# Kernel optimization log

Measured on AMD Instinct MI355X. Metric: run time of the kernel, lower is better.

## Reference

```python
import jax, jax.numpy as jnp
import numpy as np

N, E, G = 100000, 1600000, 64
IN, H, OUT = 128, 64, 16  # hidden/2 = 32
SLOPE = 0.01


def setup_inputs() -> dict:
    key = jax.random.key(0)
    ks = jax.random.split(key, 7)
    features = jax.random.normal(ks[0], (N, IN), dtype=jnp.float32)
    src = jax.random.randint(ks[1], (E,), 0, N)
    dst = jax.random.randint(ks[2], (E,), 0, N)
    graph_ids = jnp.sort(jax.random.randint(ks[3], (N,), 0, G))
    # kaiming-uniform-ish fan_in init, bias=False everywhere
    W1 = jax.random.uniform(ks[4], (IN, H), jnp.float32, -1.0, 1.0) * np.sqrt(3.0 / IN)
    W2 = jax.random.uniform(ks[5], (H, H // 2), jnp.float32, -1.0, 1.0) * np.sqrt(3.0 / H)
    Wc = jax.random.uniform(ks[6], (H // 2, OUT), jnp.float32, -1.0, 1.0) * np.sqrt(3.0 / (H // 2))
    return {"features": features, "src": src, "dst": dst, "graph_ids": graph_ids,
            "W1": W1, "W2": W2, "Wc": Wc}


def _graph_conv(x, W, src, dst, n):
    # DGL GraphConv, norm='both', bias=False:
    # out = D_in^{-1/2} A (D_out^{-1/2} x) W   (degrees clamped to >= 1)
    ones = jnp.ones(src.shape[0], dtype=x.dtype)
    outdeg = jnp.clip(jax.ops.segment_sum(ones, src, num_segments=n), 1.0)
    indeg = jnp.clip(jax.ops.segment_sum(ones, dst, num_segments=n), 1.0)
    h = (x * jax.lax.rsqrt(outdeg)[:, None]) @ W  # project first (in_dim > out_dim)
    m = jax.ops.segment_sum(h[src], dst, num_segments=n)  # sparse aggregation
    return m * jax.lax.rsqrt(indeg)[:, None]


def reference(features, src, dst, graph_ids, W1, W2, Wc):
    h = jax.nn.leaky_relu(_graph_conv(features, W1, src, dst, N), SLOPE)
    h = jax.nn.leaky_relu(_graph_conv(h, W2, src, dst, N), SLOPE)
    # dropout is identity at inference
    sums = jax.ops.segment_sum(h, graph_ids, num_segments=G)
    cnts = jnp.clip(jax.ops.segment_sum(jnp.ones((N,), h.dtype), graph_ids, num_segments=G), 1.0)
    mean = sums / cnts[:, None]  # dgl.mean_nodes
    return mean @ Wc  # [G, OUT]
```

## Files before the change

kernel.cpp:

```cpp
#include <hip/hip_runtime.h>

#define NN 100000
#define NE 1600000
#define NG 64
#define D_IN 128
#define D_H 64
#define D_H2 32
#define D_OUT 16
#define SLOPE 0.01f
#define REC 48

#define BSH 9
#define NBK 196
#define NCB 250
#define CHE (NE / NCB)
#define BCAP 9216

typedef _Float16 half2v __attribute__((ext_vector_type(2)));
typedef _Float16 h8 __attribute__((ext_vector_type(8)));
typedef float f32x4 __attribute__((ext_vector_type(4)));

__global__ __launch_bounds__(256) void p12_scatter(const int* __restrict__ src,
                                                   const int* __restrict__ dst,
                                                   int* __restrict__ gcur,
                                                   unsigned* __restrict__ pk,
                                                   unsigned short* __restrict__ srcs16) {
  __shared__ int hD[NBK], hS[NBK];
  __shared__ int cD[NBK], cS[NBK];
  int b = blockIdx.x, t = threadIdx.x;
  for (int i = t; i < NBK; i += 256) { hD[i] = 0; hS[i] = 0; }
  __syncthreads();
  const int4* s4 = (const int4*)(src + b * CHE);
  const int4* d4 = (const int4*)(dst + b * CHE);
  for (int i = t; i < CHE / 4; i += 256) {
    int4 s = s4[i], d = d4[i];
    atomicAdd(&hD[d.x >> BSH], 1); atomicAdd(&hD[d.y >> BSH], 1);
    atomicAdd(&hD[d.z >> BSH], 1); atomicAdd(&hD[d.w >> BSH], 1);
    atomicAdd(&hS[s.x >> BSH], 1); atomicAdd(&hS[s.y >> BSH], 1);
    atomicAdd(&hS[s.z >> BSH], 1); atomicAdd(&hS[s.w >> BSH], 1);
  }
  __syncthreads();
  for (int i = t; i < NBK; i += 256) {
    cD[i] = atomicAdd(&gcur[i], hD[i]);
    cS[i] = atomicAdd(&gcur[NBK + i], hS[i]);
  }
  __syncthreads();
  for (int i = t; i < CHE / 4; i += 256) {
    int4 s = s4[i], d = d4[i];
#pragma unroll
    for (int j = 0; j < 4; ++j) {
      int ss = (j == 0) ? s.x : (j == 1) ? s.y : (j == 2) ? s.z : s.w;
      int dd = (j == 0) ? d.x : (j == 1) ? d.y : (j == 2) ? d.z : d.w;
      int kd = dd >> BSH, ks = ss >> BSH;
      int pd = atomicAdd(&cD[kd], 1);
      if (pd < BCAP) pk[(size_t)kd * BCAP + pd] =
          ((unsigned)(dd & 511) << 17) | (unsigned)ss;
      int ps = atomicAdd(&cS[ks], 1);
      if (ps < BCAP) srcs16[(size_t)ks * BCAP + ps] = (unsigned short)(ss & 511);
    }
  }
}

__global__ __launch_bounds__(256) void p3_build(const unsigned* __restrict__ pk,
                                                const unsigned short* __restrict__ srcs16,
                                                const int* __restrict__ gcur,
                                                int* __restrict__ adj,
                                                int* __restrict__ indeg,
                                                int* __restrict__ outdeg) {
  __shared__ int hh[512];
  int bb = blockIdx.x, t = threadIdx.x;
  for (int i = t; i < 512; i += 256) hh[i] = 0;
  __syncthreads();
  if (bb < NBK) {
    int k = bb;
    int n0 = k << BSH;
    int lo = k * BCAP;
    int hi = lo + min(gcur[k], BCAP);
    for (int i = lo + t; i < hi; i += 256) {
      unsigned v = pk[i];
      int local = v >> 17;
      int pos = atomicAdd(&hh[local], 1);
      if (pos < REC) adj[(size_t)(n0 + local) * REC + pos] = (int)(v & 0x1FFFF);
    }
    __syncthreads();
    for (int i = t; i < 512; i += 256) {
      int n = n0 + i;
      if (n < NN) {
        int dg = hh[i];
        indeg[n] = dg;
        int d = min(dg, REC);
        int dr = min((d + 15) & ~15, REC);
        for (int j = d; j < dr; ++j) adj[(size_t)n * REC + j] = NN;
      }
    }
  } else {
    int k = bb - NBK;
    int lo = k * BCAP;
    int hi = lo + min(gcur[NBK + k], BCAP);
    for (int i = lo + t; i < hi; i += 256) atomicAdd(&hh[srcs16[i]], 1);
    __syncthreads();
    int n0 = k << BSH;
    for (int i = t; i < 512; i += 256) {
      int n = n0 + i;
      if (n < NN) outdeg[n] = hh[i];
    }
  }
}

__global__ __launch_bounds__(256) void k_mm1f(const float* __restrict__ X,
                                              const float* __restrict__ W,
                                              const int* __restrict__ odeg,
                                              _Float16* __restrict__ Y) {
  __shared__ _Float16 Wt[64][136];
  int t = threadIdx.x;
  if (blockIdx.x == 0 && t < 64) Y[(size_t)NN * 64 + t] = (_Float16)0.f;
  for (int i = t; i < 128 * 64; i += 256) {
    int k = i >> 6, f = i & 63;
    Wt[f][k] = (_Float16)W[i];
  }
  __syncthreads();
  int lane = t & 63, w = t >> 6;
  int m = lane & 15, q = lane >> 4;
  h8 bf[4][4];
#pragma unroll
  for (int kc = 0; kc < 4; ++kc)
#pragma unroll
    for (int nt = 0; nt < 4; ++nt)
      bf[kc][nt] = *(const h8*)&Wt[nt * 16 + m][kc * 32 + q * 8];

  const int NT = NN / 16;
  int idx = blockIdx.x * 4 + w;
  int t0 = idx * 2, t1 = t0 + 1;
  f32x4 r0[8], r1[8];
  if (t0 < NT) {
    const f32x4* X0 = (const f32x4*)(X + (size_t)(t0 * 16 + m) * 128);
#pragma unroll
    for (int kc = 0; kc < 4; ++kc) {
      r0[kc * 2 + 0] = X0[kc * 8 + q * 2 + 0];
      r0[kc * 2 + 1] = X0[kc * 8 + q * 2 + 1];
    }
  }
  if (t1 < NT) {
    const f32x4* X1 = (const f32x4*)(X + (size_t)(t1 * 16 + m) * 128);
#pragma unroll
    for (int kc = 0; kc < 4; ++kc) {
      r1[kc * 2 + 0] = X1[kc * 8 + q * 2 + 0];
      r1[kc * 2 + 1] = X1[kc * 8 + q * 2 + 1];
    }
  }
#pragma unroll
  for (int half = 0; half < 2; ++half) {
    int tile = (half == 0) ? t0 : t1;
    if (tile >= NT) continue;
    f32x4* rr = (half == 0) ? r0 : r1;
    f32x4 acc[4] = {{0,0,0,0},{0,0,0,0},{0,0,0,0},{0,0,0,0}};
#pragma unroll
    for (int kc = 0; kc < 4; ++kc) {
      f32x4 x0 = rr[kc * 2 + 0], x1 = rr[kc * 2 + 1];
      h8 a;
      a[0] = (_Float16)x0.x; a[1] = (_Float16)x0.y;
      a[2] = (_Float16)x0.z; a[3] = (_Float16)x0.w;
      a[4] = (_Float16)x1.x; a[5] = (_Float16)x1.y;
      a[6] = (_Float16)x1.z; a[7] = (_Float16)x1.w;
#pragma unroll
      for (int nt = 0; nt < 4; ++nt)
        acc[nt] = __builtin_amdgcn_mfma_f32_16x16x32_f16(a, bf[kc][nt], acc[nt], 0, 0, 0);
    }
    int n0 = tile * 16;
#pragma unroll
    for (int reg = 0; reg < 4; ++reg) {
      int nn = n0 + q * 4 + reg;
      float sc = rsqrtf((float)max(odeg[nn], 1));
#pragma unroll
      for (int nt = 0; nt < 4; ++nt)
        Y[(size_t)nn * 64 + nt * 16 + m] = (_Float16)(acc[nt][reg] * sc);
    }
  }
}

__global__ __launch_bounds__(256) void k_aggmm2(const int* __restrict__ adj,
                                                const int* __restrict__ indeg,
                                                const int* __restrict__ odeg,
                                                const h8* __restrict__ H8,
                                                const float* __restrict__ W,
                                                _Float16* __restrict__ Y) {
  __shared__ _Float16 Ht[32][72];
  __shared__ _Float16 Wt[32][72];
  int t = threadIdx.x;
  if (blockIdx.x == 0 && t < 32) Y[(size_t)NN * 32 + t] = (_Float16)0.f;
  for (int i = t; i < 64 * 32; i += 256) {
    int k = i >> 5, f = i & 31;
    Wt[f][k] = (_Float16)W[i];
  }
  int l8 = t & 7;
  int nd = t >> 3;
  int node = blockIdx.x * 32 + nd;
  int deg = indeg[node];
  int groups = (min(deg, REC) + 15) >> 4;
  const int4* c4 = (const int4*)(adj + (size_t)node * REC);
  float acc[8] = {0.f, 0.f, 0.f, 0.f, 0.f, 0.f, 0.f, 0.f};
  for (int g = 0; g < groups; ++g) {
    int4 ca = c4[g * 4 + 0], cb = c4[g * 4 + 1];
    {
      h8 v0 = H8[(size_t)ca.x * 8 + l8];
      h8 v1 = H8[(size_t)ca.y * 8 + l8];
      h8 v2 = H8[(size_t)ca.z * 8 + l8];
      h8 v3 = H8[(size_t)ca.w * 8 + l8];
      h8 v4 = H8[(size_t)cb.x * 8 + l8];
      h8 v5 = H8[(size_t)cb.y * 8 + l8];
      h8 v6 = H8[(size_t)cb.z * 8 + l8];
      h8 v7 = H8[(size_t)cb.w * 8 + l8];
#pragma unroll
      for (int j = 0; j < 8; ++j)
        acc[j] += (((float)v0[j] + (float)v1[j]) + ((float)v2[j] + (float)v3[j])) +
                  (((float)v4[j] + (float)v5[j]) + ((float)v6[j] + (float)v7[j]));
    }
    int4 cc = c4[g * 4 + 2], cd = c4[g * 4 + 3];
    {
      h8 v0 = H8[(size_t)cc.x * 8 + l8];
      h8 v1 = H8[(size_t)cc.y * 8 + l8];
      h8 v2 = H8[(size_t)cc.z * 8 + l8];
      h8 v3 = H8[(size_t)cc.w * 8 + l8];
      h8 v4 = H8[(size_t)cd.x * 8 + l8];
      h8 v5 = H8[(size_t)cd.y * 8 + l8];
      h8 v6 = H8[(size_t)cd.z * 8 + l8];
      h8 v7 = H8[(size_t)cd.w * 8 + l8];
#pragma unroll
      for (int j = 0; j < 8; ++j)
        acc[j] += (((float)v0[j] + (float)v1[j]) + ((float)v2[j] + (float)v3[j])) +
                  (((float)v4[j] + (float)v5[j]) + ((float)v6[j] + (float)v7[j]));
    }
  }
  float sc = rsqrtf((float)max(deg, 1));
  h8 hv;
#pragma unroll
  for (int j = 0; j < 8; ++j) {
    float x = acc[j] * sc;
    hv[j] = (_Float16)((x > 0.f) ? x : SLOPE * x);
  }
  *(h8*)&Ht[nd][l8 * 8] = hv;
  __syncthreads();
  int lane = t & 63, w = t >> 6;
  if (w < 2) {
    int m = lane & 15, q = lane >> 4;
    h8 bf[2][2];
#pragma unroll
    for (int kc = 0; kc < 2; ++kc)
#pragma unroll
      for (int nt = 0; nt < 2; ++nt)
        bf[kc][nt] = *(const h8*)&Wt[nt * 16 + m][kc * 32 + q * 8];
    h8 af[2];
#pragma unroll
    for (int kc = 0; kc < 2; ++kc)
      af[kc] = *(const h8*)&Ht[w * 16 + m][kc * 32 + q * 8];
    f32x4 acc2[2] = {{0, 0, 0, 0}, {0, 0, 0, 0}};
#pragma unroll
    for (int kc = 0; kc < 2; ++kc)
#pragma unroll
      for (int nt = 0; nt < 2; ++nt)
        acc2[nt] = __builtin_amdgcn_mfma_f32_16x16x32_f16(af[kc], bf[kc][nt], acc2[nt], 0, 0, 0);
#pragma unroll
    for (int reg = 0; reg < 4; ++reg) {
      int nn = blockIdx.x * 32 + w * 16 + q * 4 + reg;
      float sco = rsqrtf((float)max(odeg[nn], 1));
#pragma unroll
      for (int nt = 0; nt < 2; ++nt)
        Y[(size_t)nn * 32 + nt * 16 + m] = (_Float16)(acc2[nt][reg] * sco);
    }
  }
}

__global__ __launch_bounds__(256) void k_agg32v(const int* __restrict__ adj,
                                                const int* __restrict__ indeg,
                                                const h8* __restrict__ H8,
                                                h8* __restrict__ Y8) {
  int l4 = threadIdx.x & 3;
  int node = blockIdx.x * 64 + (threadIdx.x >> 2);
  if (node >= NN) return;
  int deg = indeg[node];
  int groups = (min(deg, REC) + 15) >> 4;
  const int4* c4 = (const int4*)(adj + (size_t)node * REC);
  float acc[8] = {0.f, 0.f, 0.f, 0.f, 0.f, 0.f, 0.f, 0.f};
  for (int g = 0; g < groups; ++g) {
    int4 ca = c4[g * 4 + 0], cb = c4[g * 4 + 1];
    {
      h8 v0 = H8[(size_t)ca.x * 4 + l4];
      h8 v1 = H8[(size_t)ca.y * 4 + l4];
      h8 v2 = H8[(size_t)ca.z * 4 + l4];
      h8 v3 = H8[(size_t)ca.w * 4 + l4];
      h8 v4 = H8[(size_t)cb.x * 4 + l4];
      h8 v5 = H8[(size_t)cb.y * 4 + l4];
      h8 v6 = H8[(size_t)cb.z * 4 + l4];
      h8 v7 = H8[(size_t)cb.w * 4 + l4];
#pragma unroll
      for (int j = 0; j < 8; ++j)
        acc[j] += (((float)v0[j] + (float)v1[j]) + ((float)v2[j] + (float)v3[j])) +
                  (((float)v4[j] + (float)v5[j]) + ((float)v6[j] + (float)v7[j]));
    }
    int4 cc = c4[g * 4 + 2], cd = c4[g * 4 + 3];
    {
      h8 v0 = H8[(size_t)cc.x * 4 + l4];
      h8 v1 = H8[(size_t)cc.y * 4 + l4];
      h8 v2 = H8[(size_t)cc.z * 4 + l4];
      h8 v3 = H8[(size_t)cc.w * 4 + l4];
      h8 v4 = H8[(size_t)cd.x * 4 + l4];
      h8 v5 = H8[(size_t)cd.y * 4 + l4];
      h8 v6 = H8[(size_t)cd.z * 4 + l4];
      h8 v7 = H8[(size_t)cd.w * 4 + l4];
#pragma unroll
      for (int j = 0; j < 8; ++j)
        acc[j] += (((float)v0[j] + (float)v1[j]) + ((float)v2[j] + (float)v3[j])) +
                  (((float)v4[j] + (float)v5[j]) + ((float)v6[j] + (float)v7[j]));
    }
  }
  float sc = rsqrtf((float)max(deg, 1));
  h8 o;
#pragma unroll
  for (int j = 0; j < 8; ++j) {
    float x = acc[j] * sc;
    o[j] = (_Float16)((x > 0.f) ? x : SLOPE * x);
  }
  Y8[(size_t)node * 4 + l4] = o;
}

__global__ __launch_bounds__(256) void k_poolout(const half2v* __restrict__ H2,
                                                 const int* __restrict__ gid,
                                                 const float* __restrict__ Wc,
                                                 float* __restrict__ out) {
  __shared__ float red[16][33];
  __shared__ float mean[D_H2];
  __shared__ int sb[2];
  int g = blockIdx.x, t = threadIdx.x;
  if (t < 2) {
    int target = g + t;
    int lo = 0, hi = NN;
    while (lo < hi) {
      int mid = (lo + hi) >> 1;
      if (gid[mid] < target) lo = mid + 1; else hi = mid;
    }
    sb[t] = lo;
  }
  __syncthreads();
  int start = sb[0], end = sb[1];
  int c2 = t & 15, r = t >> 4;
  float sx = 0.f, sy = 0.f;
  for (int n = start + r; n < end; n += 16) {
    half2v v = H2[(size_t)n * 16 + c2];
    sx += (float)v.x;
    sy += (float)v.y;
  }
  red[r][c2 * 2] = sx;
  red[r][c2 * 2 + 1] = sy;
  __syncthreads();
  if (r < 8) { red[r][c2 * 2] += red[r + 8][c2 * 2]; red[r][c2 * 2 + 1] += red[r + 8][c2 * 2 + 1]; }
  __syncthreads();
  if (r < 4) { red[r][c2 * 2] += red[r + 4][c2 * 2]; red[r][c2 * 2 + 1] += red[r + 4][c2 * 2 + 1]; }
  __syncthreads();
  if (r < 2) { red[r][c2 * 2] += red[r + 2][c2 * 2]; red[r][c2 * 2 + 1] += red[r + 2][c2 * 2 + 1]; }
  __syncthreads();
  if (r == 0) {
    float inv = 1.0f / (float)max(end - start, 1);
    mean[c2 * 2] = (red[0][c2 * 2] + red[1][c2 * 2]) * inv;
    mean[c2 * 2 + 1] = (red[0][c2 * 2 + 1] + red[1][c2 * 2 + 1]) * inv;
  }
  __syncthreads();
  if (t < D_OUT) {
    float acc = 0.f;
#pragma unroll
    for (int cc = 0; cc < D_H2; ++cc) acc += mean[cc] * Wc[cc * D_OUT + t];
    out[g * D_OUT + t] = acc;
  }
}

extern "C" void kernel_launch(void* const* d_in, const int* in_sizes, int n_in,
                              void* d_out, int out_size, void* d_ws, size_t ws_size,
                              hipStream_t stream) {
  const float* X  = (const float*)d_in[0];
  const int*   src = (const int*)d_in[1];
  const int*   dst = (const int*)d_in[2];
  const int*   gid = (const int*)d_in[3];
  const float* W1 = (const float*)d_in[4];
  const float* W2 = (const float*)d_in[5];
  const float* Wc = (const float*)d_in[6];
  float* out = (float*)d_out;

  char* p = (char*)d_ws;
  auto alloc = [&](size_t bytes) {
    char* q = p;
    p += (bytes + 255) & ~(size_t)255;
    return q;
  };
  int*            outdeg = (int*)alloc(NN * 4);
  int*            indeg  = (int*)alloc(NN * 4);
  int*            gcur   = (int*)alloc(2 * NBK * 4);
  unsigned*       pk     = (unsigned*)alloc((size_t)NBK * BCAP * 4);
  unsigned short* srcs16 = (unsigned short*)alloc((size_t)NBK * BCAP * 2);
  int*            adj    = (int*)alloc((size_t)NN * REC * 4);
  _Float16*       bufA   = (_Float16*)alloc((size_t)(NN + 1) * 64 * 2);
  _Float16*       bufB   = (_Float16*)alloc((size_t)(NN + 1) * 32 * 2);
  _Float16*       bufC   = (_Float16*)alloc((size_t)(NN + 1) * 32 * 2);

  hipMemsetAsync(gcur, 0, 2 * NBK * 4, stream);

  p12_scatter<<<NCB, 256, 0, stream>>>(src, dst, gcur, pk, srcs16);
  p3_build<<<2 * NBK, 256, 0, stream>>>(pk, srcs16, gcur, adj, indeg, outdeg);

  k_mm1f<<<782, 256, 0, stream>>>(X, W1, outdeg, bufA);
  k_aggmm2<<<NN / 32, 256, 0, stream>>>(adj, indeg, outdeg, (const h8*)bufA, W2, bufC);
  k_agg32v<<<(NN + 63) / 64, 256, 0, stream>>>(adj, indeg, (const h8*)bufC, (h8*)bufB);

  k_poolout<<<NG, 256, 0, stream>>>((const half2v*)bufB, gid, Wc, out);
}
```

Baseline: 237.1 us.

## Fuse second-layer aggregation with per-graph mean pooling via shared atomics

The final aggregation kernel now accumulates its leaky-ReLU outputs straight into per-graph sums. It uses LDS atomics across up to four graph slots per block, then global atomics into a small pool buffer, which removes the fp16 intermediate write and the separate pooling pass. A single-block kernel then computes means and the classifier matmul, and the pool buffer is zeroed by extending the existing memset. Separately, placeholder padding in the adjacency build now uses int4 stores. The fusion relies on sorted graph ids spanning at most four graphs per 64-node block, since it clamps otherwise, and float atomics make summation order nondeterministic.

```diff
diff --git a/kernel.cpp b/kernel.cpp
--- a/kernel.cpp
+++ b/kernel.cpp
@@ -83,6 +83,7 @@
       if (pos < REC) adj[(size_t)(n0 + local) * REC + pos] = (int)(v & 0x1FFFF);
     }
     __syncthreads();
+    int4 ph = make_int4(NN, NN, NN, NN);
     for (int i = t; i < 512; i += 256) {
       int n = n0 + i;
       if (n < NN) {
@@ -90,7 +91,9 @@
         indeg[n] = dg;
         int d = min(dg, REC);
         int dr = min((d + 15) & ~15, REC);
-        for (int j = d; j < dr; ++j) adj[(size_t)n * REC + j] = NN;
+        int j = d;
+        for (; j & 3; ++j) if (j < dr) adj[(size_t)n * REC + j] = NN;
+        for (; j + 4 <= dr; j += 4) *(int4*)&adj[(size_t)n * REC + j] = ph;
       }
     }
   } else {
@@ -270,16 +273,24 @@
   }
 }
 
-__global__ __launch_bounds__(256) void k_agg32v(const int* __restrict__ adj,
+__global__ __launch_bounds__(256) void k_agg32p(const int* __restrict__ adj,
                                                 const int* __restrict__ indeg,
+                                                const int* __restrict__ gid,
                                                 const h8* __restrict__ H8,
-                                                h8* __restrict__ Y8) {
-  int l4 = threadIdx.x & 3;
-  int node = blockIdx.x * 64 + (threadIdx.x >> 2);
-  if (node >= NN) return;
-  int deg = indeg[node];
+                                                float* __restrict__ pool) {
+  __shared__ float lp[4][D_H2];
+  __shared__ int gmin_s;
+  int t = threadIdx.x;
+  int l4 = t & 3;
+  int nd = t >> 2;
+  int node = blockIdx.x * 64 + nd;
+  bool valid = node < NN;
+  int nclamp = valid ? node : NN - 1;
+  if (t == 0) gmin_s = gid[blockIdx.x * 64];
+  for (int i = t; i < 4 * D_H2; i += 256) ((float*)lp)[i] = 0.f;
+  int deg = valid ? indeg[nclamp] : 0;
   int groups = (min(deg, REC) + 15) >> 4;
-  const int4* c4 = (const int4*)(adj + (size_t)node * REC);
+  const int4* c4 = (const int4*)(adj + (size_t)nclamp * REC);
   float acc[8] = {0.f, 0.f, 0.f, 0.f, 0.f, 0.f, 0.f, 0.f};
   for (int g = 0; g < groups; ++g) {
     int4 ca = c4[g * 4 + 0], cb = c4[g * 4 + 1];
@@ -313,62 +324,56 @@
                   (((float)v4[j] + (float)v5[j]) + ((float)v6[j] + (float)v7[j]));
     }
   }
-  float sc = rsqrtf((float)max(deg, 1));
-  h8 o;
-#pragma unroll
-  for (int j = 0; j < 8; ++j) {
-    float x = acc[j] * sc;
-    o[j] = (_Float16)((x > 0.f) ? x : SLOPE * x);
-  }
-  Y8[(size_t)node * 4 + l4] = o;
-}
-
-__global__ __launch_bounds__(256) void k_poolout(const half2v* __restrict__ H2,
-                                                 const int* __restrict__ gid,
-                                                 const float* __restrict__ Wc,
-                                                 float* __restrict__ out) {
-  __shared__ float red[16][33];
-  __shared__ float mean[D_H2];
-  __shared__ int sb[2];
-  int g = blockIdx.x, t = threadIdx.x;
-  if (t < 2) {
-    int target = g + t;
+  __syncthreads();
+  if (valid) {
+    float sc = rsqrtf((float)max(deg, 1));
+    int gl = min(gid[node] - gmin_s, 3);
+#pragma unroll
+    for (int j = 0; j < 8; ++j) {
+      float x = acc[j] * sc;
+      x = (x > 0.f) ? x : SLOPE * x;
+      atomicAdd(&lp[gl][l4 * 8 + j], x);
+    }
+  }
+  __syncthreads();
+  if (t < 4 * D_H2) {
+    float v = ((float*)lp)[t];
+    if (v != 0.f) {
+      int gl = t >> 5, f = t & 31;
+      atomicAdd(&pool[(gmin_s + gl) * D_H2 + f], v);
+    }
+  }
+}
+
+__global__ __launch_bounds__(256) void k_out(const float* __restrict__ pool,
+                                             const int* __restrict__ gid,
+                                             const float* __restrict__ Wc,
+                                             float* __restrict__ out) {
+  __shared__ int bnd[NG + 1];
+  __shared__ float mean[NG][D_H2];
+  int t = threadIdx.x;
+  if (t <= NG) {
+    int target = t;
     int lo = 0, hi = NN;
     while (lo < hi) {
       int mid = (lo + hi) >> 1;
       if (gid[mid] < target) lo = mid + 1; else hi = mid;
     }
-    sb[t] = lo;
-  }
-  __syncthreads();
-  int start = sb[0], end = sb[1];
-  int c2 = t & 15, r = t >> 4;
-  float sx = 0.f, sy = 0.f;
-  for (int n = start + r; n < end; n += 16) {
-    half2v v = H2[(size_t)n * 16 + c2];
-    sx += (float)v.x;
-    sy += (float)v.y;
-  }
-  red[r][c2 * 2] = sx;
-  red[r][c2 * 2 + 1] = sy;
-  __syncthreads();
-  if (r < 8) { red[r][c2 * 2] += red[r + 8][c2 * 2]; red[r][c2 * 2 + 1] += red[r + 8][c2 * 2 + 1]; }
-  __syncthreads();
-  if (r < 4) { red[r][c2 * 2] += red[r + 4][c2 * 2]; red[r][c2 * 2 + 1] += red[r + 4][c2 * 2 + 1]; }
-  __syncthreads();
-  if (r < 2) { red[r][c2 * 2] += red[r + 2][c2 * 2]; red[r][c2 * 2 + 1] += red[r + 2][c2 * 2 + 1]; }
-  __syncthreads();
-  if (r == 0) {
-    float inv = 1.0f / (float)max(end - start, 1);
-    mean[c2 * 2] = (red[0][c2 * 2] + red[1][c2 * 2]) * inv;
-    mean[c2 * 2 + 1] = (red[0][c2 * 2 + 1] + red[1][c2 * 2 + 1]) * inv;
-  }
-  __syncthreads();
-  if (t < D_OUT) {
-    float acc = 0.f;
-#pragma unroll
-    for (int cc = 0; cc < D_H2; ++cc) acc += mean[cc] * Wc[cc * D_OUT + t];
-    out[g * D_OUT + t] = acc;
+    bnd[t] = lo;
+  }
+  __syncthreads();
+  for (int i = t; i < NG * D_H2; i += 256) {
+    int g = i >> 5;
+    float inv = 1.0f / (float)max(bnd[g + 1] - bnd[g], 1);
+    ((float*)mean)[i] = pool[i] * inv;
+  }
+  __syncthreads();
+  for (int i = t; i < NG * D_OUT; i += 256) {
+    int g = i / D_OUT, o = i % D_OUT;
+    float s = 0.f;
+#pragma unroll
+    for (int c = 0; c < D_H2; ++c) s += mean[g][c] * Wc[c * D_OUT + o];
+    out[i] = s;
   }
 }
 
@@ -393,21 +398,20 @@
   int*            outdeg = (int*)alloc(NN * 4);
   int*            indeg  = (int*)alloc(NN * 4);
   int*            gcur   = (int*)alloc(2 * NBK * 4);
+  float*          pool   = (float*)alloc(NG * D_H2 * 4);
   unsigned*       pk     = (unsigned*)alloc((size_t)NBK * BCAP * 4);
   unsigned short* srcs16 = (unsigned short*)alloc((size_t)NBK * BCAP * 2);
   int*            adj    = (int*)alloc((size_t)NN * REC * 4);
   _Float16*       bufA   = (_Float16*)alloc((size_t)(NN + 1) * 64 * 2);
-  _Float16*       bufB   = (_Float16*)alloc((size_t)(NN + 1) * 32 * 2);
   _Float16*       bufC   = (_Float16*)alloc((size_t)(NN + 1) * 32 * 2);
 
-  hipMemsetAsync(gcur, 0, 2 * NBK * 4, stream);
+  hipMemsetAsync(gcur, 0, ((2 * NBK * 4 + 255) & ~255) + NG * D_H2 * 4, stream);
 
   p12_scatter<<<NCB, 256, 0, stream>>>(src, dst, gcur, pk, srcs16);
   p3_build<<<2 * NBK, 256, 0, stream>>>(pk, srcs16, gcur, adj, indeg, outdeg);
 
   k_mm1f<<<782, 256, 0, stream>>>(X, W1, outdeg, bufA);
   k_aggmm2<<<NN / 32, 256, 0, stream>>>(adj, indeg, outdeg, (const h8*)bufA, W2, bufC);
-  k_agg32v<<<(NN + 63) / 64, 256, 0, stream>>>(adj, indeg, (const h8*)bufC, (h8*)bufB);
-
-  k_poolout<<<NG, 256, 0, stream>>>((const half2v*)bufB, gid, Wc, out);
-}
+  k_agg32p<<<(NN + 63) / 64, 256, 0, stream>>>(adj, indeg, gid, (const h8*)bufC, pool);
+  k_out<<<1, 256, 0, stream>>>(pool, gid, Wc, out);
+}
```

Result: faster. 229.7 us (-3.1%).
